# Performance work log

Hardware: AMD Instinct MI355X
Metric: run time of the kernel (lower is better)

## Reference

```python
import jax, jax.numpy as jnp
import numpy as np

B, C, H, W = 4, 512, 128, 128
C8 = C // 8


def setup_inputs() -> dict:
    key = jax.random.key(0)
    ks = jax.random.split(key, 10)
    s = 0.02
    return {
        "x_exmplar": jax.random.normal(ks[0], (B, C, H, W), jnp.float32),
        "x_query": jax.random.normal(ks[1], (B, C, H, W), jnp.float32),
        "Wq": jax.random.normal(ks[2], (C8, C), jnp.float32) * s,
        "bq": jax.random.normal(ks[3], (C8,), jnp.float32) * s,
        "Wk": jax.random.normal(ks[4], (C8, C), jnp.float32) * s,
        "bk": jax.random.normal(ks[5], (C8,), jnp.float32) * s,
        "Wv": jax.random.normal(ks[6], (C, C), jnp.float32) * s,
        "bv": jax.random.normal(ks[7], (C,), jnp.float32) * s,
        "gamma_1": jax.random.normal(ks[8], (1,), jnp.float32) * 0.1,
        "gamma_2": jax.random.normal(ks[9], (1,), jnp.float32) * 0.1,
    }


def _conv1x1(x, Wt, b):
    # x: (B,C,H,W), Wt: (O,C) -> (B,O,H,W)
    return jnp.einsum('bchw,oc->bohw', x, Wt) + b[None, :, None, None]


def reference(x_exmplar, x_query, Wq, bq, Wk, bk, Wv, bv, gamma_1, gamma_2):
    q = _conv1x1(x_query, Wq, bq)      # (B,C8,H,W)
    k = _conv1x1(x_exmplar, Wk, bk)    # (B,C8,H,W)
    v = _conv1x1(x_exmplar, Wv, bv)    # (B,C,H,W)

    # vertical (H) path: energy_H[b,h,w,j] = sum_c q[b,c,h,w] k[b,c,j,w], -inf on h==j
    energy_H = jnp.einsum('bchw,bcjw->bhwj', q, k)
    eye = jnp.eye(H, dtype=bool)[None, :, None, :]       # (1,H,1,H)
    energy_H = jnp.where(eye, -jnp.inf, energy_H)
    # horizontal (W) path: energy_W[b,h,w,j] = sum_c q[b,c,h,w] k[b,c,h,j]
    energy_W = jnp.einsum('bchw,bchj->bhwj', q, k)

    concate = jax.nn.softmax(jnp.concatenate([energy_H, energy_W], axis=-1), axis=-1)
    att_H = concate[..., :H]           # (B,H,W,H)
    att_W = concate[..., H:]           # (B,H,W,W)

    out_H = jnp.einsum('bcjw,bhwj->bchw', v, att_H)
    out_W = jnp.einsum('bchj,bhwj->bchw', v, att_W)

    # diagonal (LR / RL) paths; D = min(H,W) = H for square maps
    q_d = jnp.diagonal(q, axis1=2, axis2=3)   # (B,C8,D)
    k_d = jnp.diagonal(k, axis1=2, axis2=3)   # (B,C8,D)
    v_d = jnp.diagonal(v, axis1=2, axis2=3)   # (B,C,D)
    # diag of transpose(2,3) with offset 0 equals diag, so LR == RL faithfully
    energy_LR = jnp.einsum('bci,bcj->bij', k_d, q_d)  # (B,D,D)
    energy_RL = energy_LR
    # softmax over a singleton trailing axis (as in the original code)
    out_LR = jax.nn.softmax(jnp.einsum('bcd,bdj->bcj', v_d, energy_LR)[..., None], axis=3)
    out_RL = jax.nn.softmax(jnp.einsum('bcd,bdj->bcj', v_d, energy_RL)[..., None], axis=3)

    out_sum = out_H + out_W + out_LR + out_RL   # (B,C,H,W) via broadcast of (B,C,D,1)
    return (gamma_1 * out_sum + x_exmplar, gamma_2 * out_sum + x_query)
```

## Files before the change

kernel.cpp:

```cpp
#include <hip/hip_runtime.h>
#include <stdint.h>

typedef unsigned short u16;
typedef __attribute__((ext_vector_type(8))) short bf16x8;
typedef __attribute__((ext_vector_type(4))) float f32x4;

#define NB   4
#define NC   512
#define NC8  64
#define NH   128
#define NW   128
#define NHW  16384

__device__ __forceinline__ float b2f(u16 u) {
  union { float f; uint32_t i; } x; x.i = ((uint32_t)u) << 16; return x.f;
}
__device__ __forceinline__ u16 f2b(float f) {
  union { float f; uint32_t u; } x; x.f = f;
  uint32_t r = x.u + 0x7FFF + ((x.u >> 16) & 1);
  return (u16)(r >> 16);
}
__device__ __forceinline__ uint4 pack8bf(const float* f) {
  uint4 u;
  u.x = (uint32_t)f2b(f[0]) | ((uint32_t)f2b(f[1]) << 16);
  u.y = (uint32_t)f2b(f[2]) | ((uint32_t)f2b(f[3]) << 16);
  u.z = (uint32_t)f2b(f[4]) | ((uint32_t)f2b(f[5]) << 16);
  u.w = (uint32_t)f2b(f[6]) | ((uint32_t)f2b(f[7]) << 16);
  return u;
}
__device__ __forceinline__ void unpack8bf(uint4 u, float* f) {
  f[0] = b2f((u16)(u.x & 0xFFFF)); f[1] = b2f((u16)(u.x >> 16));
  f[2] = b2f((u16)(u.y & 0xFFFF)); f[3] = b2f((u16)(u.y >> 16));
  f[4] = b2f((u16)(u.z & 0xFFFF)); f[5] = b2f((u16)(u.z >> 16));
  f[6] = b2f((u16)(u.w & 0xFFFF)); f[7] = b2f((u16)(u.w >> 16));
}

__global__ __launch_bounds__(256) void convert_w(const float* __restrict__ W,
                                                 u16* __restrict__ Wb) {
  int i = (blockIdx.x * 256 + threadIdx.x) * 8;
  float4 a = *reinterpret_cast<const float4*>(W + i);
  float4 b = *reinterpret_cast<const float4*>(W + i + 4);
  float f[8] = {a.x, a.y, a.z, a.w, b.x, b.y, b.z, b.w};
  *reinterpret_cast<uint4*>(Wb + i) = pack8bf(f);
}

__global__ __launch_bounds__(256) void transpose_cvt(const float* __restrict__ x,
                                                     u16* __restrict__ xT) {
  __shared__ float tile[32][33];
  int b = blockIdx.z;
  int c0 = blockIdx.y * 32;
  int n0 = blockIdx.x * 32;
  int t = threadIdx.x;
  int tx = t & 31, ty = t >> 5;
  const float* src = x + ((size_t)b * NC + c0) * NHW + n0;
  for (int k = 0; k < 4; k++)
    tile[ty + k * 8][tx] = src[(size_t)(ty + k * 8) * NHW + tx];
  __syncthreads();
  if (t < 128) {
    int n = t >> 2, cg = t & 3;
    float f[8];
    for (int j = 0; j < 8; j++) f[j] = tile[cg * 8 + j][n];
    *reinterpret_cast<uint4*>(&xT[((size_t)b * NHW + n0 + n) * NC + c0 + cg * 8]) = pack8bf(f);
  }
}

__global__ __launch_bounds__(256) void proj64_mfma(const u16* __restrict__ xT,
                                                   const u16* __restrict__ Wb,
                                                   const float* __restrict__ bias,
                                                   u16* __restrict__ yT) {
  __shared__ __align__(16) u16 smem[12288];
  char* AsB = (char*)smem;
  char* BsB = (char*)smem + 8192;
  int n0 = blockIdx.x * 128, b = blockIdx.y;
  int t = threadIdx.x;
  int wid = t >> 6, lane = t & 63;
  int wm = wid >> 1, wn = wid & 1;
  int l15 = lane & 15, lhi = lane >> 4;

  f32x4 acc[2][4];
#pragma unroll
  for (int m = 0; m < 2; m++)
#pragma unroll
    for (int n = 0; n < 4; n++)
#pragma unroll
      for (int r = 0; r < 4; r++) acc[m][n][r] = 0.f;

  const u16* Bbase = xT + ((size_t)b * NHW + n0) * NC;

  for (int c0 = 0; c0 < NC; c0 += 64) {
#pragma unroll
    for (int p = 0; p < 2; p++) {
      int idx = t + p * 256;
      int row = idx >> 3, cb = (idx & 7) * 8;
      int dst = row * 128 + ((cb * 2) ^ ((row & 7) << 4));
      bf16x8 av = *reinterpret_cast<const bf16x8*>(Wb + (size_t)row * NC + c0 + cb);
      *reinterpret_cast<bf16x8*>(AsB + dst) = av;
    }
#pragma unroll
    for (int p = 0; p < 4; p++) {
      int idx = t + p * 256;
      int row = idx >> 3, cb = (idx & 7) * 8;
      int dst = row * 128 + ((cb * 2) ^ ((row & 7) << 4));
      bf16x8 bv = *reinterpret_cast<const bf16x8*>(Bbase + (size_t)row * NC + c0 + cb);
      *reinterpret_cast<bf16x8*>(BsB + dst) = bv;
    }
    __syncthreads();
#pragma unroll
    for (int kk = 0; kk < 2; kk++) {
      int kbyte = kk * 64 + lhi * 16;
      bf16x8 af[2], bfr[4];
#pragma unroll
      for (int m = 0; m < 2; m++) {
        int row = wm * 32 + m * 16 + l15;
        af[m] = *reinterpret_cast<const bf16x8*>(AsB + row * 128 + (kbyte ^ ((row & 7) << 4)));
      }
#pragma unroll
      for (int n = 0; n < 4; n++) {
        int row = wn * 64 + n * 16 + l15;
        bfr[n] = *reinterpret_cast<const bf16x8*>(BsB + row * 128 + (kbyte ^ ((row & 7) << 4)));
      }
#pragma unroll
      for (int m = 0; m < 2; m++)
#pragma unroll
        for (int n = 0; n < 4; n++)
          acc[m][n] = __builtin_amdgcn_mfma_f32_16x16x32_bf16(af[m], bfr[n], acc[m][n], 0, 0, 0);
    }
    __syncthreads();
  }

  char* stage = (char*)smem;
#pragma unroll
  for (int m = 0; m < 2; m++) {
#pragma unroll
    for (int r = 0; r < 4; r++) {
      int o = wm * 32 + m * 16 + lhi * 4 + r;
      float bval = bias[o];
#pragma unroll
      for (int n = 0; n < 4; n++) {
        int col = wn * 64 + n * 16 + l15;
        int byte = col * 128 + ((o * 2) ^ ((col & 7) << 4));
        *reinterpret_cast<u16*>(stage + byte) = f2b(acc[m][n][r] + bval);
      }
    }
  }
  __syncthreads();
#pragma unroll
  for (int p = 0; p < 4; p++) {
    int idx = t + p * 256;
    int col = idx >> 3, seg = idx & 7;
    int byte = col * 128 + ((seg * 16) ^ ((col & 7) << 4));
    uint4 v = *reinterpret_cast<const uint4*>(stage + byte);
    *reinterpret_cast<uint4*>(&yT[((size_t)b * NHW + n0 + col) * 64 + seg * 8]) = v;
  }
}

__global__ __launch_bounds__(256) void proj_v_mfma(const u16* __restrict__ xT,
                                                   const u16* __restrict__ Wb,
                                                   const float* __restrict__ bias,
                                                   u16* __restrict__ y) {
  __shared__ __align__(16) u16 smem[16384];
  char* AsB = (char*)smem;
  char* BsB = (char*)(smem + 8192);
  int o0 = blockIdx.x * 128, n0 = blockIdx.y * 128, b = blockIdx.z;
  int t = threadIdx.x;
  int wid = t >> 6, lane = t & 63;
  int wm = wid >> 1, wn = wid & 1;
  int l15 = lane & 15, lhi = lane >> 4;

  f32x4 acc[4][4];
#pragma unroll
  for (int m = 0; m < 4; m++)
#pragma unroll
    for (int n = 0; n < 4; n++)
#pragma unroll
      for (int r = 0; r < 4; r++) acc[m][n][r] = 0.f;

  const u16* Arow = Wb + (size_t)o0 * NC;
  const u16* Brow = xT + ((size_t)b * NHW + n0) * NC;

  for (int c0 = 0; c0 < NC; c0 += 64) {
#pragma unroll
    for (int p = 0; p < 4; p++) {
      int idx = t + p * 256;
      int row = idx >> 3;
      int cb  = (idx & 7) * 8;
      int dst = row * 128 + ((cb * 2) ^ ((row & 7) << 4));
      bf16x8 av = *reinterpret_cast<const bf16x8*>(Arow + (size_t)row * NC + c0 + cb);
      *reinterpret_cast<bf16x8*>(AsB + dst) = av;
      bf16x8 bv = *reinterpret_cast<const bf16x8*>(Brow + (size_t)row * NC + c0 + cb);
      *reinterpret_cast<bf16x8*>(BsB + dst) = bv;
    }
    __syncthreads();
#pragma unroll
    for (int kk = 0; kk < 2; kk++) {
      int kbyte = kk * 64 + lhi * 16;
      bf16x8 af[4], bfr[4];
#pragma unroll
      for (int m = 0; m < 4; m++) {
        int row = wm * 64 + m * 16 + l15;
        af[m] = *reinterpret_cast<const bf16x8*>(AsB + row * 128 + (kbyte ^ ((row & 7) << 4)));
      }
#pragma unroll
      for (int n = 0; n < 4; n++) {
        int row = wn * 64 + n * 16 + l15;
        bfr[n] = *reinterpret_cast<const bf16x8*>(BsB + row * 128 + (kbyte ^ ((row & 7) << 4)));
      }
#pragma unroll
      for (int m = 0; m < 4; m++)
#pragma unroll
        for (int n = 0; n < 4; n++)
          acc[m][n] = __builtin_amdgcn_mfma_f32_16x16x32_bf16(af[m], bfr[n], acc[m][n], 0, 0, 0);
    }
    __syncthreads();
  }

  char* stage = (char*)smem + wid * 8192;
#pragma unroll
  for (int m = 0; m < 4; m++) {
#pragma unroll
    for (int r = 0; r < 4; r++) {
      int lrow = m * 16 + lhi * 4 + r;
      float bval = bias[o0 + wm * 64 + lrow];
#pragma unroll
      for (int n = 0; n < 4; n++) {
        int col = n * 16 + l15;
        *reinterpret_cast<u16*>(stage + lrow * 128 + col * 2) = f2b(acc[m][n][r] + bval);
      }
    }
  }
  __syncthreads();
#pragma unroll
  for (int s = 0; s < 8; s++) {
    int row  = s * 8 + (lane >> 3);
    int colb = (lane & 7) * 8;
    uint4 v = *reinterpret_cast<const uint4*>(stage + row * 128 + colb * 2);
    size_t addr = ((size_t)b * NC + o0 + wm * 64 + row) * (size_t)NHW + n0 + wn * 64 + colb;
    *reinterpret_cast<uint4*>(&y[addr]) = v;
  }
}

__global__ __launch_bounds__(256) void transpose128(const u16* __restrict__ src,
                                                    u16* __restrict__ dst) {
  __shared__ u16 tile[32][33];
  int p = blockIdx.z;
  int i0 = blockIdx.y * 32, j0 = blockIdx.x * 32;
  int tx = threadIdx.x & 31, ty = threadIdx.x >> 5;
  const u16* s = src + (size_t)p * NHW;
  u16* d = dst + (size_t)p * NHW;
  for (int k = 0; k < 4; k++) {
    int i = i0 + ty + k * 8;
    tile[ty + k * 8][tx] = s[(size_t)i * 128 + j0 + tx];
  }
  __syncthreads();
  for (int k = 0; k < 4; k++) {
    int j = j0 + ty + k * 8;
    d[(size_t)j * 128 + i0 + tx] = tile[tx][ty + k * 8];
  }
}

__global__ __launch_bounds__(256) void energy_mfma(const u16* __restrict__ QT,
                                                   const u16* __restrict__ KT,
                                                   u16* __restrict__ att, int isH) {
  __shared__ __align__(16) u16 smem[16384];
  char* AsB = (char*)smem;
  char* BsB = (char*)(smem + 8192);
  int s = blockIdx.x, b = blockIdx.y;
  int t = threadIdx.x;
  int wid = t >> 6, lane = t & 63;
  int wm = wid >> 1, wn = wid & 1;
  int l15 = lane & 15, lhi = lane >> 4;

  size_t base = (size_t)b * NHW * 64;
  size_t rowstride = isH ? (size_t)128 * 64 : 64;
  size_t off0 = isH ? (size_t)s * 64 : (size_t)s * 128 * 64;

  f32x4 acc[4][4];
#pragma unroll
  for (int m = 0; m < 4; m++)
#pragma unroll
    for (int n = 0; n < 4; n++)
#pragma unroll
      for (int r = 0; r < 4; r++) acc[m][n][r] = 0.f;

#pragma unroll
  for (int p = 0; p < 4; p++) {
    int idx = t + p * 256;
    int row = idx >> 3;
    int cb  = (idx & 7) * 8;
    int dst = row * 128 + ((cb * 2) ^ ((row & 7) << 4));
    bf16x8 av = *reinterpret_cast<const bf16x8*>(QT + base + off0 + (size_t)row * rowstride + cb);
    *reinterpret_cast<bf16x8*>(AsB + dst) = av;
    bf16x8 bv = *reinterpret_cast<const bf16x8*>(KT + base + off0 + (size_t)row * rowstride + cb);
    *reinterpret_cast<bf16x8*>(BsB + dst) = bv;
  }
  __syncthreads();
#pragma unroll
  for (int kk = 0; kk < 2; kk++) {
    int kbyte = kk * 64 + lhi * 16;
    bf16x8 af[4], bfr[4];
#pragma unroll
    for (int m = 0; m < 4; m++) {
      int row = wm * 64 + m * 16 + l15;
      af[m] = *reinterpret_cast<const bf16x8*>(AsB + row * 128 + (kbyte ^ ((row & 7) << 4)));
    }
#pragma unroll
    for (int n = 0; n < 4; n++) {
      int row = wn * 64 + n * 16 + l15;
      bfr[n] = *reinterpret_cast<const bf16x8*>(BsB + row * 128 + (kbyte ^ ((row & 7) << 4)));
    }
#pragma unroll
    for (int m = 0; m < 4; m++)
#pragma unroll
      for (int n = 0; n < 4; n++)
        acc[m][n] = __builtin_amdgcn_mfma_f32_16x16x32_bf16(af[m], bfr[n], acc[m][n], 0, 0, 0);
  }
  __syncthreads();

  char* stage = (char*)smem + wid * 8192;
#pragma unroll
  for (int m = 0; m < 4; m++) {
#pragma unroll
    for (int r = 0; r < 4; r++) {
      int lrow = m * 16 + lhi * 4 + r;
      int grow = wm * 64 + lrow;
#pragma unroll
      for (int n = 0; n < 4; n++) {
        int col = n * 16 + l15;
        int gcol = wn * 64 + col;
        float v = acc[m][n][r];
        if (isH && gcol == grow) v = -1e30f;
        *reinterpret_cast<u16*>(stage + lrow * 128 + col * 2) = f2b(v);
      }
    }
  }
  __syncthreads();
  size_t attb = (size_t)b * 4194304;
#pragma unroll
  for (int sb = 0; sb < 8; sb++) {
    int row  = wm * 64 + sb * 8 + (lane >> 3);
    int colb = wn * 64 + (lane & 7) * 8;
    uint4 v = *reinterpret_cast<const uint4*>(stage + (sb * 8 + (lane >> 3)) * 128 + (lane & 7) * 16);
    size_t addr = attb + (isH ? ((size_t)row * 32768 + (size_t)s * 256 + colb)
                              : ((size_t)s * 32768 + (size_t)row * 256 + 128 + colb));
    *reinterpret_cast<uint4*>(&att[addr]) = v;
  }
}

__global__ __launch_bounds__(256) void softmax_kern(u16* __restrict__ att) {
  int wave = threadIdx.x >> 6;
  int lane = threadIdx.x & 63;
  size_t row = (size_t)blockIdx.x * 4 + wave;
  u16* p = att + row * 256;
  uint2 u = *reinterpret_cast<const uint2*>(&p[lane * 4]);
  float v[4];
  v[0] = b2f((u16)(u.x & 0xFFFF)); v[1] = b2f((u16)(u.x >> 16));
  v[2] = b2f((u16)(u.y & 0xFFFF)); v[3] = b2f((u16)(u.y >> 16));
  float mx = fmaxf(fmaxf(v[0], v[1]), fmaxf(v[2], v[3]));
  for (int off = 32; off; off >>= 1) mx = fmaxf(mx, __shfl_xor(mx, off));
  float sum = 0.f;
  for (int i = 0; i < 4; i++) { v[i] = __expf(v[i] - mx); sum += v[i]; }
  for (int off = 32; off; off >>= 1) sum += __shfl_xor(sum, off);
  float inv = 1.f / sum;
  uint2 o;
  o.x = (uint32_t)f2b(v[0] * inv) | ((uint32_t)f2b(v[1] * inv) << 16);
  o.y = (uint32_t)f2b(v[2] * inv) | ((uint32_t)f2b(v[3] * inv) << 16);
  *reinterpret_cast<uint2*>(&p[lane * 4]) = o;
}

__global__ __launch_bounds__(256) void out_gemm_mfma(const u16* __restrict__ V,
                                                     const u16* __restrict__ att,
                                                     u16* __restrict__ out, int isH) {
  __shared__ __align__(16) u16 smem[16384];
  char* AsB = (char*)smem;
  char* BsB = (char*)(smem + 8192);
  int ct = blockIdx.x, s = blockIdx.y, b = blockIdx.z;
  int t = threadIdx.x;
  int wid = t >> 6, lane = t & 63;
  int wm = wid >> 1, wn = wid & 1;
  int l15 = lane & 15, lhi = lane >> 4;

  f32x4 acc[4][4];
#pragma unroll
  for (int m = 0; m < 4; m++)
#pragma unroll
    for (int n = 0; n < 4; n++)
#pragma unroll
      for (int r = 0; r < 4; r++) acc[m][n][r] = 0.f;

  const u16* Abase = V + ((size_t)(b * NC + ct * 128)) * NHW + (size_t)s * 128;
  size_t attb = (size_t)b * 4194304;
  size_t bbase = attb + (isH ? (size_t)s * 256 : (size_t)s * 32768 + 128);
  size_t bstride = isH ? 32768 : 256;

  for (int c0 = 0; c0 < 128; c0 += 64) {
#pragma unroll
    for (int p = 0; p < 4; p++) {
      int idx = t + p * 256;
      int row = idx >> 3;
      int cb  = (idx & 7) * 8;
      int dst = row * 128 + ((cb * 2) ^ ((row & 7) << 4));
      bf16x8 av = *reinterpret_cast<const bf16x8*>(Abase + (size_t)row * NHW + c0 + cb);
      *reinterpret_cast<bf16x8*>(AsB + dst) = av;
      bf16x8 bv = *reinterpret_cast<const bf16x8*>(att + bbase + (size_t)row * bstride + c0 + cb);
      *reinterpret_cast<bf16x8*>(BsB + dst) = bv;
    }
    __syncthreads();
#pragma unroll
    for (int kk = 0; kk < 2; kk++) {
      int kbyte = kk * 64 + lhi * 16;
      bf16x8 af[4], bfr[4];
#pragma unroll
      for (int m = 0; m < 4; m++) {
        int row = wm * 64 + m * 16 + l15;
        af[m] = *reinterpret_cast<const bf16x8*>(AsB + row * 128 + (kbyte ^ ((row & 7) << 4)));
      }
#pragma unroll
      for (int n = 0; n < 4; n++) {
        int row = wn * 64 + n * 16 + l15;
        bfr[n] = *reinterpret_cast<const bf16x8*>(BsB + row * 128 + (kbyte ^ ((row & 7) << 4)));
      }
#pragma unroll
      for (int m = 0; m < 4; m++)
#pragma unroll
        for (int n = 0; n < 4; n++)
          acc[m][n] = __builtin_amdgcn_mfma_f32_16x16x32_bf16(af[m], bfr[n], acc[m][n], 0, 0, 0);
    }
    __syncthreads();
  }

  char* stage = (char*)smem + wid * 8192;
#pragma unroll
  for (int m = 0; m < 4; m++) {
#pragma unroll
    for (int r = 0; r < 4; r++) {
      int lrow = m * 16 + lhi * 4 + r;
#pragma unroll
      for (int n = 0; n < 4; n++) {
        int col = n * 16 + l15;
        *reinterpret_cast<u16*>(stage + lrow * 128 + col * 2) = f2b(acc[m][n][r]);
      }
    }
  }
  __syncthreads();
#pragma unroll
  for (int sb = 0; sb < 8; sb++) {
    int row  = sb * 8 + (lane >> 3);
    int colb = (lane & 7) * 8;
    uint4 v = *reinterpret_cast<const uint4*>(stage + row * 128 + colb * 2);
    size_t addr = ((size_t)(b * NC + ct * 128 + wm * 64 + row)) * NHW + (size_t)s * 128 + wn * 64 + colb;
    *reinterpret_cast<uint4*>(&out[addr]) = v;
  }
}

__global__ __launch_bounds__(256) void epilogue(const u16* __restrict__ outWbf,
                                                const u16* __restrict__ outHsw,
                                                const float* __restrict__ xe,
                                                const float* __restrict__ xq,
                                                const float* __restrict__ g1p,
                                                const float* __restrict__ g2p,
                                                float* __restrict__ out0,
                                                float* __restrict__ out1) {
  __shared__ float tile[32][65];
  int p = blockIdx.z;
  int h0 = blockIdx.y * 64, w0 = blockIdx.x * 32;
  int t = threadIdx.x;
  {
    int w = t >> 3, hc = t & 7;
    uint4 v = *reinterpret_cast<const uint4*>(
        &outHsw[(size_t)p * NHW + (size_t)(w0 + w) * 128 + h0 + hc * 8]);
    float f[8]; unpack8bf(v, f);
    for (int j = 0; j < 8; j++) tile[w][hc * 8 + j] = f[j];
  }
  __syncthreads();
  float g1 = g1p[0], g2 = g2p[0];
  int h = t >> 2, wc = t & 3;
  size_t idx = (size_t)p * NHW + (size_t)(h0 + h) * 128 + w0 + wc * 8;
  uint4 wv = *reinterpret_cast<const uint4*>(&outWbf[idx]);
  float s[8]; unpack8bf(wv, s);
  float4 xe0 = *reinterpret_cast<const float4*>(&xe[idx]);
  float4 xe1 = *reinterpret_cast<const float4*>(&xe[idx + 4]);
  float4 xq0 = *reinterpret_cast<const float4*>(&xq[idx]);
  float4 xq1 = *reinterpret_cast<const float4*>(&xq[idx + 4]);
  float sum[8];
  for (int j = 0; j < 8; j++) sum[j] = s[j] + tile[wc * 8 + j][h] + 2.0f;
  float4 o0a = {g1 * sum[0] + xe0.x, g1 * sum[1] + xe0.y, g1 * sum[2] + xe0.z, g1 * sum[3] + xe0.w};
  float4 o0b = {g1 * sum[4] + xe1.x, g1 * sum[5] + xe1.y, g1 * sum[6] + xe1.z, g1 * sum[7] + xe1.w};
  float4 o1a = {g2 * sum[0] + xq0.x, g2 * sum[1] + xq0.y, g2 * sum[2] + xq0.z, g2 * sum[3] + xq0.w};
  float4 o1b = {g2 * sum[4] + xq1.x, g2 * sum[5] + xq1.y, g2 * sum[6] + xq1.z, g2 * sum[7] + xq1.w};
  *reinterpret_cast<float4*>(&out0[idx])     = o0a;
  *reinterpret_cast<float4*>(&out0[idx + 4]) = o0b;
  *reinterpret_cast<float4*>(&out1[idx])     = o1a;
  *reinterpret_cast<float4*>(&out1[idx + 4]) = o1b;
}

extern "C" void kernel_launch(void* const* d_in, const int* in_sizes, int n_in,
                              void* d_out, int out_size, void* d_ws, size_t ws_size,
                              hipStream_t stream) {
  (void)in_sizes; (void)n_in; (void)out_size; (void)ws_size;
  const float* xe = (const float*)d_in[0];
  const float* xq = (const float*)d_in[1];
  const float* Wq = (const float*)d_in[2];
  const float* bq = (const float*)d_in[3];
  const float* Wk = (const float*)d_in[4];
  const float* bk = (const float*)d_in[5];
  const float* Wv = (const float*)d_in[6];
  const float* bv = (const float*)d_in[7];
  const float* g1 = (const float*)d_in[8];
  const float* g2 = (const float*)d_in[9];
  float* out = (float*)d_out;

  char* ws = (char*)d_ws;
  u16* qT    = (u16*)(ws + 0);
  u16* kT    = (u16*)(ws + 8388608);
  u16* wv_bf = (u16*)(ws + 16777216);
  u16* wq_bf = (u16*)(ws + 17301504);
  u16* wk_bf = (u16*)(ws + 17367040);
  u16* v_n   = (u16*)(ws + 33554432);
  u16* v_sw  = (u16*)(ws + 100663296);
  u16* att   = (u16*)(ws + 167772160);
  u16* xT    = (u16*)(ws + 201326592);

  convert_w<<<dim3(128), 256, 0, stream>>>(Wv, wv_bf);
  convert_w<<<dim3(16), 256, 0, stream>>>(Wq, wq_bf);
  convert_w<<<dim3(16), 256, 0, stream>>>(Wk, wk_bf);
  transpose_cvt<<<dim3(512, 16, 4), 256, 0, stream>>>(xe, xT);
  proj64_mfma<<<dim3(128, 4), 256, 0, stream>>>(xT, wk_bf, bk, kT);
  proj_v_mfma<<<dim3(4, 128, 4), 256, 0, stream>>>(xT, wv_bf, bv, v_n);
  transpose_cvt<<<dim3(512, 16, 4), 256, 0, stream>>>(xq, xT);
  proj64_mfma<<<dim3(128, 4), 256, 0, stream>>>(xT, wq_bf, bq, qT);
  transpose128<<<dim3(4, 4, 2048), 256, 0, stream>>>(v_n, v_sw);
  energy_mfma<<<dim3(128, 4), 256, 0, stream>>>(qT, kT, att, 0);
  energy_mfma<<<dim3(128, 4), 256, 0, stream>>>(qT, kT, att, 1);
  softmax_kern<<<dim3(16384), 256, 0, stream>>>(att);
  out_gemm_mfma<<<dim3(4, 128, 4), 256, 0, stream>>>(v_n, att, v_n, 0);
  out_gemm_mfma<<<dim3(4, 128, 4), 256, 0, stream>>>(v_sw, att, v_sw, 1);
  epilogue<<<dim3(4, 2, 2048), 256, 0, stream>>>(v_n, v_sw, xe, xq, g1, g2,
                                                 out, out + 33554432);
}
```

Before: 771.0 us.

## Merge paired kernel launches and vectorize transposes and softmax

Several pairs of launches are folded into one grid each: the weight conversions, the two input transposes, the Q/K projections, the H/W energy GEMMs and the H/W output GEMMs. The transposes move to 64x64 tiles with float4/uint4 global accesses, and softmax now processes 8 bf16 per lane with a 32-lane reduction. The query transpose buffer is aliased onto the v_sw region to save workspace, which depends on the launch order staying as it is. The aim is to cut launch and tail overhead and to make the memory-bound transpose and softmax passes more efficient. The new LDS transpose reads may hit bank conflicts.

```diff
diff --git a/kernel.cpp b/kernel.cpp
--- a/kernel.cpp
+++ b/kernel.cpp
@@ -35,43 +35,71 @@
   f[6] = b2f((u16)(u.w & 0xFFFF)); f[7] = b2f((u16)(u.w >> 16));
 }
 
-__global__ __launch_bounds__(256) void convert_w(const float* __restrict__ W,
-                                                 u16* __restrict__ Wb) {
-  int i = (blockIdx.x * 256 + threadIdx.x) * 8;
+__global__ __launch_bounds__(256) void convert_w3(const float* __restrict__ Wv,
+                                                  const float* __restrict__ Wq,
+                                                  const float* __restrict__ Wk,
+                                                  u16* __restrict__ wv,
+                                                  u16* __restrict__ wq,
+                                                  u16* __restrict__ wk) {
+  int bid = blockIdx.x;
+  const float* W; u16* Wb; int base;
+  if (bid < 128)      { W = Wv; Wb = wv; base = bid; }
+  else if (bid < 144) { W = Wq; Wb = wq; base = bid - 128; }
+  else                { W = Wk; Wb = wk; base = bid - 144; }
+  int i = (base * 256 + threadIdx.x) * 8;
   float4 a = *reinterpret_cast<const float4*>(W + i);
   float4 b = *reinterpret_cast<const float4*>(W + i + 4);
   float f[8] = {a.x, a.y, a.z, a.w, b.x, b.y, b.z, b.w};
   *reinterpret_cast<uint4*>(Wb + i) = pack8bf(f);
 }
 
-__global__ __launch_bounds__(256) void transpose_cvt(const float* __restrict__ x,
-                                                     u16* __restrict__ xT) {
-  __shared__ float tile[32][33];
-  int b = blockIdx.z;
-  int c0 = blockIdx.y * 32;
-  int n0 = blockIdx.x * 32;
-  int t = threadIdx.x;
-  int tx = t & 31, ty = t >> 5;
+__global__ __launch_bounds__(256) void transpose_cvt2(const float* __restrict__ xe,
+                                                      const float* __restrict__ xq,
+                                                      u16* __restrict__ xeT,
+                                                      u16* __restrict__ xqT) {
+  __shared__ float tile[64][68];
+  int z = blockIdx.z;
+  int b = z & 3;
+  const float* x = (z < 4) ? xe : xq;
+  u16* xT = (z < 4) ? xeT : xqT;
+  int c0 = blockIdx.y * 64, n0 = blockIdx.x * 64;
+  int t = threadIdx.x;
   const float* src = x + ((size_t)b * NC + c0) * NHW + n0;
-  for (int k = 0; k < 4; k++)
-    tile[ty + k * 8][tx] = src[(size_t)(ty + k * 8) * NHW + tx];
-  __syncthreads();
-  if (t < 128) {
-    int n = t >> 2, cg = t & 3;
+  int r = t >> 2, cq = (t & 3) * 16;
+#pragma unroll
+  for (int v = 0; v < 4; v++) {
+    float4 f = *reinterpret_cast<const float4*>(&src[(size_t)r * NHW + cq + v * 4]);
+    *reinterpret_cast<float4*>(&tile[r][cq + v * 4]) = f;
+  }
+  __syncthreads();
+  int n = t >> 2, cg = (t & 3) * 16;
+  u16* dst = &xT[((size_t)b * NHW + n0 + n) * NC + c0 + cg];
+#pragma unroll
+  for (int half = 0; half < 2; half++) {
     float f[8];
-    for (int j = 0; j < 8; j++) f[j] = tile[cg * 8 + j][n];
-    *reinterpret_cast<uint4*>(&xT[((size_t)b * NHW + n0 + n) * NC + c0 + cg * 8]) = pack8bf(f);
-  }
-}
-
-__global__ __launch_bounds__(256) void proj64_mfma(const u16* __restrict__ xT,
-                                                   const u16* __restrict__ Wb,
-                                                   const float* __restrict__ bias,
-                                                   u16* __restrict__ yT) {
+#pragma unroll
+    for (int j = 0; j < 8; j++) f[j] = tile[cg + half * 8 + j][n];
+    *reinterpret_cast<uint4*>(dst + half * 8) = pack8bf(f);
+  }
+}
+
+__global__ __launch_bounds__(256) void proj64_qk(const u16* __restrict__ xeT,
+                                                 const u16* __restrict__ xqT,
+                                                 const u16* __restrict__ wk,
+                                                 const u16* __restrict__ wq,
+                                                 const float* __restrict__ bk,
+                                                 const float* __restrict__ bq,
+                                                 u16* __restrict__ kT,
+                                                 u16* __restrict__ qT) {
   __shared__ __align__(16) u16 smem[12288];
   char* AsB = (char*)smem;
   char* BsB = (char*)smem + 8192;
-  int n0 = blockIdx.x * 128, b = blockIdx.y;
+  int which = blockIdx.y;
+  const u16* xT = which ? xqT : xeT;
+  const u16* Wb = which ? wq : wk;
+  const float* bias = which ? bq : bk;
+  u16* yT = which ? qT : kT;
+  int n0 = blockIdx.x * 128, b = blockIdx.z;
   int t = threadIdx.x;
   int wid = t >> 6, lane = t & 63;
   int wm = wid >> 1, wn = wid & 1;
@@ -239,32 +267,46 @@
   }
 }
 
-__global__ __launch_bounds__(256) void transpose128(const u16* __restrict__ src,
-                                                    u16* __restrict__ dst) {
-  __shared__ u16 tile[32][33];
+__global__ __launch_bounds__(256) void transpose128v(const u16* __restrict__ src,
+                                                     u16* __restrict__ dst) {
+  __shared__ u16 tile[64][68];
   int p = blockIdx.z;
-  int i0 = blockIdx.y * 32, j0 = blockIdx.x * 32;
-  int tx = threadIdx.x & 31, ty = threadIdx.x >> 5;
+  int i0 = blockIdx.y * 64, j0 = blockIdx.x * 64;
+  int t = threadIdx.x;
   const u16* s = src + (size_t)p * NHW;
   u16* d = dst + (size_t)p * NHW;
-  for (int k = 0; k < 4; k++) {
-    int i = i0 + ty + k * 8;
-    tile[ty + k * 8][tx] = s[(size_t)i * 128 + j0 + tx];
-  }
-  __syncthreads();
-  for (int k = 0; k < 4; k++) {
-    int j = j0 + ty + k * 8;
-    d[(size_t)j * 128 + i0 + tx] = tile[tx][ty + k * 8];
-  }
-}
-
-__global__ __launch_bounds__(256) void energy_mfma(const u16* __restrict__ QT,
-                                                   const u16* __restrict__ KT,
-                                                   u16* __restrict__ att, int isH) {
+#pragma unroll
+  for (int q = 0; q < 2; q++) {
+    int idx = t + q * 256;
+    int r = idx >> 3, c8 = (idx & 7) * 8;
+    uint4 v = *reinterpret_cast<const uint4*>(&s[(size_t)(i0 + r) * 128 + j0 + c8]);
+    *reinterpret_cast<uint2*>(&tile[r][c8])     = make_uint2(v.x, v.y);
+    *reinterpret_cast<uint2*>(&tile[r][c8 + 4]) = make_uint2(v.z, v.w);
+  }
+  __syncthreads();
+#pragma unroll
+  for (int q = 0; q < 2; q++) {
+    int idx = t + q * 256;
+    int j = idx >> 3, c8 = (idx & 7) * 8;
+    u16 f[8];
+#pragma unroll
+    for (int v = 0; v < 8; v++) f[v] = tile[c8 + v][j];
+    uint4 o;
+    o.x = (uint32_t)f[0] | ((uint32_t)f[1] << 16);
+    o.y = (uint32_t)f[2] | ((uint32_t)f[3] << 16);
+    o.z = (uint32_t)f[4] | ((uint32_t)f[5] << 16);
+    o.w = (uint32_t)f[6] | ((uint32_t)f[7] << 16);
+    *reinterpret_cast<uint4*>(&d[(size_t)(j0 + j) * 128 + i0 + c8]) = o;
+  }
+}
+
+__global__ __launch_bounds__(256) void energy2(const u16* __restrict__ QT,
+                                               const u16* __restrict__ KT,
+                                               u16* __restrict__ att) {
   __shared__ __align__(16) u16 smem[16384];
   char* AsB = (char*)smem;
   char* BsB = (char*)(smem + 8192);
-  int s = blockIdx.x, b = blockIdx.y;
+  int s = blockIdx.x, b = blockIdx.y, isH = blockIdx.z;
   int t = threadIdx.x;
   int wid = t >> 6, lane = t & 63;
   int wm = wid >> 1, wn = wid & 1;
@@ -347,33 +389,33 @@
 }
 
 __global__ __launch_bounds__(256) void softmax_kern(u16* __restrict__ att) {
-  int wave = threadIdx.x >> 6;
-  int lane = threadIdx.x & 63;
-  size_t row = (size_t)blockIdx.x * 4 + wave;
+  int half = threadIdx.x >> 5;
+  int lane = threadIdx.x & 31;
+  size_t row = (size_t)blockIdx.x * 8 + half;
   u16* p = att + row * 256;
-  uint2 u = *reinterpret_cast<const uint2*>(&p[lane * 4]);
-  float v[4];
-  v[0] = b2f((u16)(u.x & 0xFFFF)); v[1] = b2f((u16)(u.x >> 16));
-  v[2] = b2f((u16)(u.y & 0xFFFF)); v[3] = b2f((u16)(u.y >> 16));
-  float mx = fmaxf(fmaxf(v[0], v[1]), fmaxf(v[2], v[3]));
-  for (int off = 32; off; off >>= 1) mx = fmaxf(mx, __shfl_xor(mx, off));
+  uint4 u = *reinterpret_cast<const uint4*>(&p[lane * 8]);
+  float v[8]; unpack8bf(u, v);
+  float mx = v[0];
+  for (int i = 1; i < 8; i++) mx = fmaxf(mx, v[i]);
+  for (int off = 16; off; off >>= 1) mx = fmaxf(mx, __shfl_xor(mx, off));
   float sum = 0.f;
-  for (int i = 0; i < 4; i++) { v[i] = __expf(v[i] - mx); sum += v[i]; }
-  for (int off = 32; off; off >>= 1) sum += __shfl_xor(sum, off);
+  for (int i = 0; i < 8; i++) { v[i] = __expf(v[i] - mx); sum += v[i]; }
+  for (int off = 16; off; off >>= 1) sum += __shfl_xor(sum, off);
   float inv = 1.f / sum;
-  uint2 o;
-  o.x = (uint32_t)f2b(v[0] * inv) | ((uint32_t)f2b(v[1] * inv) << 16);
-  o.y = (uint32_t)f2b(v[2] * inv) | ((uint32_t)f2b(v[3] * inv) << 16);
-  *reinterpret_cast<uint2*>(&p[lane * 4]) = o;
-}
-
-__global__ __launch_bounds__(256) void out_gemm_mfma(const u16* __restrict__ V,
-                                                     const u16* __restrict__ att,
-                                                     u16* __restrict__ out, int isH) {
+  for (int i = 0; i < 8; i++) v[i] *= inv;
+  *reinterpret_cast<uint4*>(&p[lane * 8]) = pack8bf(v);
+}
+
+__global__ __launch_bounds__(256) void out_gemm2(const u16* __restrict__ Vn,
+                                                 const u16* __restrict__ Vsw,
+                                                 const u16* __restrict__ att) {
   __shared__ __align__(16) u16 smem[16384];
   char* AsB = (char*)smem;
   char* BsB = (char*)(smem + 8192);
-  int ct = blockIdx.x, s = blockIdx.y, b = blockIdx.z;
+  int ct = blockIdx.x, s = blockIdx.y;
+  int b = blockIdx.z & 3, isH = blockIdx.z >> 2;
+  const u16* V = isH ? Vsw : Vn;
+  u16* out = const_cast<u16*>(V);
   int t = threadIdx.x;
   int wid = t >> 6, lane = t & 63;
   int wm = wid >> 1, wn = wid & 1;
@@ -518,22 +560,17 @@
   u16* v_n   = (u16*)(ws + 33554432);
   u16* v_sw  = (u16*)(ws + 100663296);
   u16* att   = (u16*)(ws + 167772160);
-  u16* xT    = (u16*)(ws + 201326592);
-
-  convert_w<<<dim3(128), 256, 0, stream>>>(Wv, wv_bf);
-  convert_w<<<dim3(16), 256, 0, stream>>>(Wq, wq_bf);
-  convert_w<<<dim3(16), 256, 0, stream>>>(Wk, wk_bf);
-  transpose_cvt<<<dim3(512, 16, 4), 256, 0, stream>>>(xe, xT);
-  proj64_mfma<<<dim3(128, 4), 256, 0, stream>>>(xT, wk_bf, bk, kT);
-  proj_v_mfma<<<dim3(4, 128, 4), 256, 0, stream>>>(xT, wv_bf, bv, v_n);
-  transpose_cvt<<<dim3(512, 16, 4), 256, 0, stream>>>(xq, xT);
-  proj64_mfma<<<dim3(128, 4), 256, 0, stream>>>(xT, wq_bf, bq, qT);
-  transpose128<<<dim3(4, 4, 2048), 256, 0, stream>>>(v_n, v_sw);
-  energy_mfma<<<dim3(128, 4), 256, 0, stream>>>(qT, kT, att, 0);
-  energy_mfma<<<dim3(128, 4), 256, 0, stream>>>(qT, kT, att, 1);
-  softmax_kern<<<dim3(16384), 256, 0, stream>>>(att);
-  out_gemm_mfma<<<dim3(4, 128, 4), 256, 0, stream>>>(v_n, att, v_n, 0);
-  out_gemm_mfma<<<dim3(4, 128, 4), 256, 0, stream>>>(v_sw, att, v_sw, 1);
+  u16* xeT   = (u16*)(ws + 201326592);
+  u16* xqT   = (u16*)(ws + 100663296);
+
+  convert_w3<<<dim3(160), 256, 0, stream>>>(Wv, Wq, Wk, wv_bf, wq_bf, wk_bf);
+  transpose_cvt2<<<dim3(256, 8, 8), 256, 0, stream>>>(xe, xq, xeT, xqT);
+  proj64_qk<<<dim3(128, 2, 4), 256, 0, stream>>>(xeT, xqT, wk_bf, wq_bf, bk, bq, kT, qT);
+  proj_v_mfma<<<dim3(4, 128, 4), 256, 0, stream>>>(xeT, wv_bf, bv, v_n);
+  transpose128v<<<dim3(2, 2, 2048), 256, 0, stream>>>(v_n, v_sw);
+  energy2<<<dim3(128, 4, 2), 256, 0, stream>>>(qT, kT, att);
+  softmax_kern<<<dim3(8192), 256, 0, stream>>>(att);
+  out_gemm2<<<dim3(4, 128, 8), 256, 0, stream>>>(v_n, v_sw, att);
   epilogue<<<dim3(4, 2, 2048), 256, 0, stream>>>(v_n, v_sw, xe, xq, g1, g2,
                                                  out, out + 33554432);
 }
```

New measurement: 748.2 us. 1.03x faster.
